# Optimization experiments

Hardware: AMD Instinct MI355X
Metric: run time of the kernel (lower is better)

## Reference

```python
import jax, jax.numpy as jnp
import numpy as np

D_MODEL = 1024; D_STATE = 128; D_CONV = 4; EXPAND = 2; HEADDIM = 64; NGROUPS = 1
CHUNK = 256; B_SZ = 2; SEQ = 4096
D_INNER = EXPAND * D_MODEL
NHEADS = D_INNER // HEADDIM
CONV_DIM = D_INNER + 2 * NGROUPS * D_STATE
D_IN_PROJ = 2 * D_INNER + 2 * NGROUPS * D_STATE + NHEADS
EPS = 1e-5


def setup_inputs() -> dict:
    key = jax.random.key(0)
    ks = jax.random.split(key, 12)
    # dt_bias init exactly as in the module (inverse-softplus of dt in [dt_min, dt_max])
    dt0 = jnp.exp(jax.random.uniform(ks[0], (NHEADS,)) * (np.log(0.1) - np.log(0.001)) + np.log(0.001))
    dt0 = jnp.clip(dt0, 1e-4)
    dt_bias = dt0 + jnp.log(-jnp.expm1(-dt0))
    A_log = jnp.log(jax.random.uniform(ks[1], (NHEADS,), minval=1.0, maxval=16.0))
    return {
        "u": jax.random.normal(ks[2], (B_SZ, SEQ, D_MODEL), jnp.float32),
        "delta_t": jax.random.uniform(ks[3], (B_SZ, SEQ, 1), jnp.float32),
        "W_in": jax.random.normal(ks[4], (D_IN_PROJ, D_MODEL), jnp.float32) / np.sqrt(D_MODEL),
        "conv_w": jax.random.normal(ks[5], (CONV_DIM, D_CONV), jnp.float32) * 0.2,
        "conv_b": jax.random.normal(ks[6], (CONV_DIM,), jnp.float32) * 0.02,
        "dt_bias": dt_bias,
        "gamma": jax.random.uniform(ks[7], (NHEADS,)),
        "A_log": A_log,
        "D": jnp.ones((NHEADS,), jnp.float32),
        "norm_w": jnp.ones((D_INNER,), jnp.float32),
        "W_out": jax.random.normal(ks[8], (D_MODEL, D_INNER), jnp.float32) / np.sqrt(D_INNER),
    }


def _segsum(x):
    # x: (..., T) -> (..., T, T) masked lower-triangular segment sums
    T = x.shape[-1]
    cs = jnp.cumsum(x, axis=-1)
    seg = cs[..., :, None] - cs[..., None, :]
    mask = jnp.tril(jnp.ones((T, T), bool))
    return jnp.where(mask, seg, -jnp.inf)


def _forward(u, delta_t, W_in, conv_w, conv_b, dt_bias, gamma, A_log, D, norm_w, W_out):
    b, L, _ = u.shape
    zxbcdt = u @ W_in.T                               # (b, L, d_in_proj), d_mlp == 0
    z = zxbcdt[..., :D_INNER]
    xBC = zxbcdt[..., D_INNER:D_INNER + CONV_DIM]
    dt = zxbcdt[..., D_INNER + CONV_DIM:]             # (b, L, nheads)
    dt = dt + gamma[None, None, :] * delta_t          # time-scale-aware shift
    # causal depthwise conv1d (pad left d_conv-1) + SiLU
    xBC = jax.lax.conv_general_dilated(
        xBC.transpose(0, 2, 1), conv_w[:, None, :], (1,), [(D_CONV - 1, 0)],
        feature_group_count=CONV_DIM, dimension_numbers=("NCH", "OIH", "NCH"))
    xBC = jax.nn.silu(xBC.transpose(0, 2, 1) + conv_b)
    x = xBC[..., :D_INNER].reshape(b, L, NHEADS, HEADDIM)
    Bm = xBC[..., D_INNER:D_INNER + D_STATE]          # ngroups == 1 -> (b, L, n)
    Cm = xBC[..., D_INNER + D_STATE:]
    A = -jnp.exp(A_log)                               # (h,)
    dt = jax.nn.softplus(dt + dt_bias)                # dt_softplus=True, dt_limit=(0, inf)
    # ---- chunked SSD scan (mamba_chunk_scan_combined) ----
    c = L // CHUNK
    Xc = (x * dt[..., None]).reshape(b, c, CHUNK, NHEADS, HEADDIM)
    Ac = (dt * A).reshape(b, c, CHUNK, NHEADS).transpose(0, 3, 1, 2)    # (b,h,c,Q)
    Bc = Bm.reshape(b, c, CHUNK, D_STATE)
    Cc = Cm.reshape(b, c, CHUNK, D_STATE)
    A_cumsum = jnp.cumsum(Ac, axis=-1)                                   # (b,h,c,Q)
    Lmat = jnp.exp(_segsum(Ac))                                          # (b,h,c,Q,Q)
    # intra-chunk (diagonal blocks)
    Y_diag = jnp.einsum("bcqn,bckn,bhcqk,bckhp->bcqhp", Cc, Bc, Lmat, Xc)
    # per-chunk states at chunk ends
    decay_states = jnp.exp(A_cumsum[..., -1:] - A_cumsum)                # (b,h,c,Q)
    states = jnp.einsum("bckn,bhck,bckhp->bchpn", Bc, decay_states, Xc)
    # inter-chunk recurrence over chunk index
    chunk_decay = jnp.exp(A_cumsum[..., -1])                             # (b,h,c)

    def step(s, inp):
        dec, st = inp
        return dec[..., None, None] * s + st, s

    _, prev_states = jax.lax.scan(
        step,
        jnp.zeros((b, NHEADS, HEADDIM, D_STATE), Xc.dtype),
        (chunk_decay.transpose(2, 0, 1), states.transpose(1, 0, 2, 3, 4)))  # prev: (c,b,h,p,n)
    Y_off = jnp.einsum("bcqn,cbhpn,bhcq->bcqhp", Cc, prev_states, jnp.exp(A_cumsum))
    y = (Y_diag + Y_off).reshape(b, L, NHEADS, HEADDIM)
    y = y + x * D[None, None, :, None]                # skip connection D
    y = y.reshape(b, L, D_INNER)
    # gated RMSNorm (norm_before_gate=False): norm(y * silu(z)) * w, group_size = d_ssm
    yg = y * jax.nn.silu(z)
    yg = yg * jax.lax.rsqrt(jnp.mean(jnp.square(yg), axis=-1, keepdims=True) + EPS) * norm_w
    return yg @ W_out.T


def reference(u, delta_t, W_in, conv_w, conv_b, dt_bias, gamma, A_log, D, norm_w, W_out):
    return _forward(u, delta_t, W_in, conv_w, conv_b, dt_bias, gamma, A_log, D, norm_w, W_out)
```

## Files before the change

kernel.cpp:

```cpp
#include <hip/hip_runtime.h>
#include <hip/hip_bf16.h>
#include <math.h>

#define DM    1024
#define DIP   4384
#define NP1   4480
#define NPX   4352
#define DI    2048
#define CD    2304
#define NH    32
#define HD    64
#define DS    128
#define CH    256
#define NCH   16
#define BSZ   2
#define SEQ   4096
#define NTOK  (BSZ*SEQ)

typedef __bf16 bf16_t;
typedef __attribute__((ext_vector_type(8))) __bf16 bf16x8;
typedef __attribute__((ext_vector_type(4))) float f32x4;

__device__ __forceinline__ f32x4 mfma16(bf16x8 a, bf16x8 b, f32x4 c) {
    return __builtin_amdgcn_mfma_f32_16x16x32_bf16(a, b, c, 0, 0, 0);
}

__device__ __forceinline__ void gload_lds16(const bf16_t* g, bf16_t* l) {
    __builtin_amdgcn_global_load_lds(
        (const __attribute__((address_space(1))) unsigned int*)g,
        (__attribute__((address_space(3))) unsigned int*)l, 16, 0, 0);
}

#define CVT_U   (NTOK * DM)
#define CVT_WI  (NP1 * DM)
#define CVT_WO  (DM * DI)
__global__ void k_cvt_all(const float* __restrict__ u, const float* __restrict__ wi,
                          const float* __restrict__ wo,
                          bf16_t* __restrict__ u_bf, bf16_t* __restrict__ wi_bf,
                          bf16_t* __restrict__ wo_bf) {
    int i = blockIdx.x * 256 + threadIdx.x;
    if (i < CVT_U) {
        u_bf[i] = (bf16_t)u[i];
    } else if (i < CVT_U + CVT_WI) {
        int j = i - CVT_U;
        int r = j >> 10;
        wi_bf[j] = (r < DIP) ? (bf16_t)wi[j] : (bf16_t)0.f;
    } else if (i < CVT_U + CVT_WI + CVT_WO) {
        int j = i - CVT_U - CVT_WI;
        wo_bf[j] = (bf16_t)wo[j];
    }
}

template <typename OutT>
__global__ __launch_bounds__(256) void k_gemm(const bf16_t* __restrict__ A,
                                              const bf16_t* __restrict__ Bt,
                                              OutT* __restrict__ C, int K, int ldc) {
    __shared__ __align__(16) bf16_t sA[128 * 32];
    __shared__ __align__(16) bf16_t sB[128 * 32];
    int tid = threadIdx.x, wave = tid >> 6, lane = tid & 63;
    int l15 = lane & 15, quad = lane >> 4;
    int m0 = blockIdx.y * 128, n0 = blockIdx.x * 128;
    int wm = (wave & 1) * 64, wn = (wave >> 1) * 64;
    f32x4 acc[4][4];
#pragma unroll
    for (int i = 0; i < 4; i++)
#pragma unroll
        for (int j = 0; j < 4; j++) acc[i][j] = (f32x4){0.f, 0.f, 0.f, 0.f};

    int srow = lane >> 2, sc = lane & 3;
    int scol = (sc ^ ((srow >> 1) & 3)) * 8;
    const bf16_t* Ag0 = A + (size_t)(m0 + wave * 32 + srow) * K + scol;
    const bf16_t* Ag1 = Ag0 + (size_t)16 * K;
    const bf16_t* Bg0 = Bt + (size_t)(n0 + wave * 32 + srow) * K + scol;
    const bf16_t* Bg1 = Bg0 + (size_t)16 * K;
    bf16_t* lA0 = sA + (wave * 32) * 32;
    bf16_t* lA1 = sA + (wave * 32 + 16) * 32;
    bf16_t* lB0 = sB + (wave * 32) * 32;
    bf16_t* lB1 = sB + (wave * 32 + 16) * 32;
    int rchunk = (quad ^ ((l15 >> 1) & 3)) * 8;

    for (int k0 = 0; k0 < K; k0 += 32) {
        gload_lds16(Ag0 + k0, lA0);
        gload_lds16(Ag1 + k0, lA1);
        gload_lds16(Bg0 + k0, lB0);
        gload_lds16(Bg1 + k0, lB1);
        __syncthreads();
        bf16x8 af[4], bg[4];
#pragma unroll
        for (int mt = 0; mt < 4; mt++) af[mt] = *(const bf16x8*)&sA[(wm + mt * 16 + l15) * 32 + rchunk];
#pragma unroll
        for (int nt = 0; nt < 4; nt++) bg[nt] = *(const bf16x8*)&sB[(wn + nt * 16 + l15) * 32 + rchunk];
#pragma unroll
        for (int mt = 0; mt < 4; mt++)
#pragma unroll
            for (int nt = 0; nt < 4; nt++)
                acc[mt][nt] = mfma16(af[mt], bg[nt], acc[mt][nt]);
        __syncthreads();
    }
#pragma unroll
    for (int mt = 0; mt < 4; mt++)
#pragma unroll
        for (int nt = 0; nt < 4; nt++)
#pragma unroll
            for (int r = 0; r < 4; r++)
                C[(size_t)(m0 + wm + mt * 16 + quad * 4 + r) * ldc + n0 + wn + nt * 16 + l15] =
                    (OutT)acc[mt][nt][r];
}

#define WPAD 1032
__global__ __launch_bounds__(256) void k_dtgemm(const bf16_t* __restrict__ A,
                                                const bf16_t* __restrict__ Wdt,
                                                float* __restrict__ dtf) {
    __shared__ __align__(16) bf16_t sW[32 * WPAD];
    __shared__ __align__(16) bf16_t sA[128 * 32];
    int tid = threadIdx.x, wave = tid >> 6, lane = tid & 63;
    int l15 = lane & 15, quad = lane >> 4;
    int m0 = blockIdx.x * 128;
#pragma unroll
    for (int it = 0; it < 16; it++) {
        int idx = it * 2048 + tid * 8;
        int r = idx >> 10, c = idx & 1023;
        *(bf16x8*)&sW[r * WPAD + c] = *(const bf16x8*)(Wdt + (size_t)r * DM + c);
    }
    f32x4 acc[2][2];
#pragma unroll
    for (int i = 0; i < 2; i++)
#pragma unroll
        for (int j = 0; j < 2; j++) acc[i][j] = (f32x4){0.f, 0.f, 0.f, 0.f};

    int srow = lane >> 2, sc = lane & 3;
    int scol = (sc ^ ((srow >> 1) & 3)) * 8;
    const bf16_t* Ag0 = A + (size_t)(m0 + wave * 32 + srow) * DM + scol;
    const bf16_t* Ag1 = Ag0 + (size_t)16 * DM;
    bf16_t* lA0 = sA + (wave * 32) * 32;
    bf16_t* lA1 = sA + (wave * 32 + 16) * 32;
    int rchunk = (quad ^ ((l15 >> 1) & 3)) * 8;

    for (int k0 = 0; k0 < DM; k0 += 32) {
        gload_lds16(Ag0 + k0, lA0);
        gload_lds16(Ag1 + k0, lA1);
        __syncthreads();
        bf16x8 af[2], bg[2];
#pragma unroll
        for (int mt = 0; mt < 2; mt++)
            af[mt] = *(const bf16x8*)&sA[(wave * 32 + mt * 16 + l15) * 32 + rchunk];
#pragma unroll
        for (int nt = 0; nt < 2; nt++)
            bg[nt] = *(const bf16x8*)&sW[(nt * 16 + l15) * WPAD + k0 + quad * 8];
#pragma unroll
        for (int mt = 0; mt < 2; mt++)
#pragma unroll
            for (int nt = 0; nt < 2; nt++)
                acc[mt][nt] = mfma16(af[mt], bg[nt], acc[mt][nt]);
        __syncthreads();
    }
#pragma unroll
    for (int mt = 0; mt < 2; mt++)
#pragma unroll
        for (int nt = 0; nt < 2; nt++)
#pragma unroll
            for (int r = 0; r < 4; r++)
                dtf[(size_t)(m0 + wave * 32 + mt * 16 + quad * 4 + r) * NH + nt * 16 + l15] =
                    acc[mt][nt][r];
}

__global__ __launch_bounds__(256) void k_dtcum(const float* __restrict__ dtf,
                                               const float* __restrict__ delta_t,
                                               const float* __restrict__ gamma,
                                               const float* __restrict__ dt_bias,
                                               const float* __restrict__ A_log,
                                               float* __restrict__ dtb, float* __restrict__ acum) {
    int blk = blockIdx.x;
    int h = blk & (NH - 1), bc = blk >> 5;
    int q = threadIdx.x;
    size_t tok = (size_t)bc * CH + q;
    float x = dtf[tok * NH + h] + gamma[h] * delta_t[tok] + dt_bias[h];
    float dt = (x > 20.f) ? x : log1pf(expf(x));
    float Ah = -expf(A_log[h]);
    __shared__ __align__(16) float s[CH];
    s[q] = dt * Ah;
    __syncthreads();
#pragma unroll
    for (int off = 1; off < CH; off <<= 1) {
        float v = (q >= off) ? s[q - off] : 0.f;
        __syncthreads();
        s[q] += v;
        __syncthreads();
    }
    dtb[(size_t)blk * CH + q] = dt;
    acum[(size_t)blk * CH + q] = s[q];
}

__global__ __launch_bounds__(256) void k_conv(const bf16_t* __restrict__ zxp,
                                              const float* __restrict__ cw,
                                              const float* __restrict__ cb,
                                              bf16_t* __restrict__ xBC) {
    int ch = blockIdx.x * 256 + threadIdx.x;
    int tok0 = blockIdx.y * 8;
    int l0 = tok0 & (SEQ - 1);
    float w0 = cw[ch * 4], w1 = cw[ch * 4 + 1], w2 = cw[ch * 4 + 2], w3 = cw[ch * 4 + 3];
    float bias = cb[ch];
    float h0 = 0.f, h1 = 0.f, h2 = 0.f;
    if (l0 != 0) {
        h0 = (float)zxp[(size_t)(tok0 - 3) * NPX + ch];
        h1 = (float)zxp[(size_t)(tok0 - 2) * NPX + ch];
        h2 = (float)zxp[(size_t)(tok0 - 1) * NPX + ch];
    }
#pragma unroll
    for (int j = 0; j < 8; j++) {
        float cur = (float)zxp[(size_t)(tok0 + j) * NPX + ch];
        float acc = bias + h0 * w0 + h1 * w1 + h2 * w2 + cur * w3;
        float sv = acc / (1.f + expf(-acc));
        xBC[(size_t)(tok0 + j) * CD + ch] = (bf16_t)sv;
        h0 = h1; h1 = h2; h2 = cur;
    }
}

__global__ __launch_bounds__(256) void k_trans(const bf16_t* __restrict__ xBC,
                                               const float* __restrict__ dtb,
                                               bf16_t* __restrict__ Xt, bf16_t* __restrict__ Btr) {
    int t = blockIdx.x, bc = blockIdx.y, tid = threadIdx.x;
    __shared__ __align__(16) bf16_t tile[CH][72];
    __shared__ __align__(16) float sdt[CH];
    int chbase = (t < 32) ? t * 64 : DI + (t - 32) * 64;
#pragma unroll
    for (int pp = 0; pp < 8; pp++) {
        int q = pp * 32 + (tid >> 3), col = (tid & 7) * 8;
        *(bf16x8*)&tile[q][col] = *(const bf16x8*)(xBC + (size_t)(bc * CH + q) * CD + chbase + col);
    }
    if (t < 32) sdt[tid] = dtb[(size_t)(bc * NH + t) * CH + tid];
    __syncthreads();
    int pl = tid >> 2, qg = tid & 3;
#pragma unroll
    for (int c8 = 0; c8 < 8; c8++) {
        int q0 = qg * 64 + c8 * 8;
        bf16x8 v;
        if (t < 32) {
#pragma unroll
            for (int j = 0; j < 8; j++) v[j] = (bf16_t)((float)tile[q0 + j][pl] * sdt[q0 + j]);
            size_t row = (size_t)(bc * NH + t) * 64 + pl;
            *(bf16x8*)(Xt + row * CH + q0) = v;
        } else {
#pragma unroll
            for (int j = 0; j < 8; j++) v[j] = tile[q0 + j][pl];
            size_t row = (size_t)bc * DS + (t - 32) * 64 + pl;
            *(bf16x8*)(Btr + row * CH + q0) = v;
        }
    }
}

__global__ __launch_bounds__(256) void k_states(const bf16_t* __restrict__ Xt,
                                                const bf16_t* __restrict__ Btr,
                                                const float* __restrict__ acum,
                                                bf16_t* __restrict__ states) {
    int blk = blockIdx.x;
    int bc = blk >> 5;
    int tid = threadIdx.x, wave = tid >> 6, lane = tid & 63;
    int l15 = lane & 15, quad = lane >> 4;
    __shared__ __align__(16) float sdec[CH];
    {
        size_t base = (size_t)blk * CH;
        float al = acum[base + CH - 1];
        sdec[tid] = __expf(al - acum[base + tid]);
    }
    __syncthreads();
    const bf16_t* Xb = Xt + (size_t)blk * 64 * CH;
    const bf16_t* Bb = Btr + (size_t)bc * DS * CH;
    f32x4 acc[4][2];
#pragma unroll
    for (int i = 0; i < 4; i++)
#pragma unroll
        for (int j = 0; j < 2; j++) acc[i][j] = (f32x4){0.f, 0.f, 0.f, 0.f};
#pragma unroll
    for (int ks = 0; ks < 8; ks++) {
        float d0[8];
#pragma unroll
        for (int j = 0; j < 8; j++) d0[j] = sdec[ks * 32 + quad * 8 + j];
        bf16x8 a[4], b[2];
#pragma unroll
        for (int mt = 0; mt < 4; mt++) {
            bf16x8 raw = *(const bf16x8*)(Xb + (size_t)(mt * 16 + l15) * CH + ks * 32 + quad * 8);
#pragma unroll
            for (int j = 0; j < 8; j++) a[mt][j] = (bf16_t)((float)raw[j] * d0[j]);
        }
#pragma unroll
        for (int nt = 0; nt < 2; nt++)
            b[nt] = *(const bf16x8*)(Bb + (size_t)(wave * 32 + nt * 16 + l15) * CH + ks * 32 + quad * 8);
#pragma unroll
        for (int mt = 0; mt < 4; mt++)
#pragma unroll
            for (int nt = 0; nt < 2; nt++)
                acc[mt][nt] = mfma16(a[mt], b[nt], acc[mt][nt]);
    }
#pragma unroll
    for (int mt = 0; mt < 4; mt++)
#pragma unroll
        for (int nt = 0; nt < 2; nt++)
#pragma unroll
            for (int r = 0; r < 4; r++)
                states[(size_t)blk * 64 * DS + (size_t)(mt * 16 + quad * 4 + r) * DS + wave * 32 + nt * 16 + l15] =
                    (bf16_t)acc[mt][nt][r];
}

__global__ __launch_bounds__(256) void k_scan(const bf16_t* __restrict__ states,
                                              const float* __restrict__ acum,
                                              bf16_t* __restrict__ prevb) {
    int blk = blockIdx.x;
    int bh = blk >> 5;
    int b = bh >> 5, h = bh & 31;
    int e = (blk & 31) * 256 + threadIdx.x;
    float prev = 0.f;
    for (int c = 0; c < NCH; c++) {
        size_t idx = (size_t)(b * NCH + c) * NH + h;
        float dec = __expf(acum[idx * CH + CH - 1]);
        size_t i = idx * 64 * DS + e;
        prevb[i] = (bf16_t)prev;
        prev = prev * dec + (float)states[i];
    }
}

__global__ __launch_bounds__(256) void k_sgen(const bf16_t* __restrict__ xBC,
                                              bf16_t* __restrict__ Sraw) {
    int t = blockIdx.x, bc = blockIdx.y;
    int qt = (t == 0) ? 1 : (t < 3) ? 2 : 3;
    int kt = t - qt * (qt - 1) / 2;
    int tid = threadIdx.x, wave = tid >> 6, lane = tid & 63;
    int l15 = lane & 15, quad = lane >> 4;
    const bf16_t* Cbase = xBC + (size_t)bc * CH * CD + DI + DS;
    const bf16_t* Bbase = xBC + (size_t)bc * CH * CD + DI;
    f32x4 acc[4];
#pragma unroll
    for (int j = 0; j < 4; j++) acc[j] = (f32x4){0.f, 0.f, 0.f, 0.f};
#pragma unroll
    for (int ks = 0; ks < 4; ks++) {
        bf16x8 a = *(const bf16x8*)(Cbase + (size_t)(qt * 64 + wave * 16 + l15) * CD + ks * 32 + quad * 8);
        bf16x8 b[4];
#pragma unroll
        for (int nt = 0; nt < 4; nt++)
            b[nt] = *(const bf16x8*)(Bbase + (size_t)(kt * 64 + nt * 16 + l15) * CD + ks * 32 + quad * 8);
#pragma unroll
        for (int nt = 0; nt < 4; nt++) acc[nt] = mfma16(a, b[nt], acc[nt]);
    }
    bf16_t* out = Sraw + ((size_t)bc * 6 + t) * 64 * 64;
#pragma unroll
    for (int nt = 0; nt < 4; nt++)
#pragma unroll
        for (int r = 0; r < 4; r++)
            out[(size_t)(wave * 16 + quad * 4 + r) * 64 + nt * 16 + l15] = (bf16_t)acc[nt][r];
}

__global__ __launch_bounds__(256) void k_chunky(const bf16_t* __restrict__ xBC,
                                                const bf16_t* __restrict__ Xt,
                                                const bf16_t* __restrict__ prevb,
                                                const bf16_t* __restrict__ Sraw,
                                                const float* __restrict__ acum,
                                                const float* __restrict__ Dp,
                                                bf16_t* __restrict__ yf) {
    int blk = blockIdx.x;
    int bc = blk >> 5, h = blk & 31;
    int tid = threadIdx.x, wave = tid >> 6, lane = tid & 63;
    int l15 = lane & 15, quad = lane >> 4;
    __shared__ __align__(16) float sac[CH];
    __shared__ __align__(16) bf16_t sS[4][64][72];
    sac[tid] = acum[(size_t)blk * CH + tid];
    __syncthreads();

    const bf16_t* Cbase = xBC + (size_t)bc * CH * CD + DI + DS;
    const bf16_t* Bbase = xBC + (size_t)bc * CH * CD + DI;
    const bf16_t* XtB = Xt + (size_t)blk * 64 * CH;
    const bf16_t* pvB = prevb + (size_t)blk * 64 * DS;

    int qw = wave * 64;
    float refq = sac[qw];
    float s_ref = __expf(refq);
    f32x4 acc[4][4];
#pragma unroll
    for (int i = 0; i < 4; i++)
#pragma unroll
        for (int j = 0; j < 4; j++) acc[i][j] = (f32x4){0.f, 0.f, 0.f, 0.f};

#pragma unroll
    for (int ks = 0; ks < 4; ks++) {
        bf16x8 a[4], b[4];
#pragma unroll
        for (int mt = 0; mt < 4; mt++)
            a[mt] = *(const bf16x8*)(Cbase + (size_t)(qw + mt * 16 + l15) * CD + ks * 32 + quad * 8);
#pragma unroll
        for (int nt = 0; nt < 4; nt++)
            b[nt] = *(const bf16x8*)(pvB + (size_t)(nt * 16 + l15) * DS + ks * 32 + quad * 8);
#pragma unroll
        for (int mt = 0; mt < 4; mt++)
#pragma unroll
            for (int nt = 0; nt < 4; nt++)
                acc[mt][nt] = mfma16(a[mt], b[nt], acc[mt][nt]);
    }
#pragma unroll
    for (int mt = 0; mt < 4; mt++)
#pragma unroll
        for (int nt = 0; nt < 4; nt++)
#pragma unroll
            for (int r = 0; r < 4; r++) acc[mt][nt][r] *= s_ref;

    for (int kt = 0; kt < wave; kt++) {
        const bf16_t* St = Sraw + ((size_t)bc * 6 + wave * (wave - 1) / 2 + kt) * 64 * 64;
#pragma unroll
        for (int ks = 0; ks < 2; ks++) {
            float ekv[8];
#pragma unroll
            for (int j = 0; j < 8; j++)
                ekv[j] = __expf(refq - sac[kt * 64 + ks * 32 + quad * 8 + j]);
            bf16x8 a[4], b[4];
#pragma unroll
            for (int mt = 0; mt < 4; mt++)
                a[mt] = *(const bf16x8*)(St + (size_t)(mt * 16 + l15) * 64 + ks * 32 + quad * 8);
#pragma unroll
            for (int nt = 0; nt < 4; nt++) {
                bf16x8 raw = *(const bf16x8*)(XtB + (size_t)(nt * 16 + l15) * CH + kt * 64 + ks * 32 + quad * 8);
#pragma unroll
                for (int j = 0; j < 8; j++) b[nt][j] = (bf16_t)((float)raw[j] * ekv[j]);
            }
#pragma unroll
            for (int mt = 0; mt < 4; mt++)
#pragma unroll
                for (int nt = 0; nt < 4; nt++)
                    acc[mt][nt] = mfma16(a[mt], b[nt], acc[mt][nt]);
        }
    }

    float sacq[4][4];
#pragma unroll
    for (int mt = 0; mt < 4; mt++)
#pragma unroll
        for (int r = 0; r < 4; r++) sacq[mt][r] = sac[qw + mt * 16 + quad * 4 + r];
#pragma unroll
    for (int mt = 0; mt < 4; mt++) {
        float eqv[4];
#pragma unroll
        for (int r = 0; r < 4; r++) eqv[r] = __expf(sacq[mt][r] - refq);
#pragma unroll
        for (int nt = 0; nt < 4; nt++)
#pragma unroll
            for (int r = 0; r < 4; r++) acc[mt][nt][r] *= eqv[r];
    }

    {
        int kt = wave;
        f32x4 s2[4][4];
#pragma unroll
        for (int i = 0; i < 4; i++)
#pragma unroll
            for (int j = 0; j < 4; j++) s2[i][j] = (f32x4){0.f, 0.f, 0.f, 0.f};
#pragma unroll
        for (int ks = 0; ks < 4; ks++) {
            bf16x8 a[4], b[4];
#pragma unroll
            for (int mt = 0; mt < 4; mt++)
                a[mt] = *(const bf16x8*)(Cbase + (size_t)(qw + mt * 16 + l15) * CD + ks * 32 + quad * 8);
#pragma unroll
            for (int nt = 0; nt < 4; nt++)
                b[nt] = *(const bf16x8*)(Bbase + (size_t)(kt * 64 + nt * 16 + l15) * CD + ks * 32 + quad * 8);
#pragma unroll
            for (int mt = 0; mt < 4; mt++)
#pragma unroll
                for (int nt = 0; nt < 4; nt++)
                    s2[mt][nt] = mfma16(a[mt], b[nt], s2[mt][nt]);
        }
        float sack[4];
#pragma unroll
        for (int nt = 0; nt < 4; nt++) sack[nt] = sac[kt * 64 + nt * 16 + l15];
#pragma unroll
        for (int mt = 0; mt < 4; mt++)
#pragma unroll
            for (int nt = 0; nt < 4; nt++) {
                int kp = kt * 64 + nt * 16 + l15;
#pragma unroll
                for (int r = 0; r < 4; r++) {
                    int lq = mt * 16 + quad * 4 + r;
                    int q = qw + lq;
                    float v = (kp <= q) ? s2[mt][nt][r] * __expf(sacq[mt][r] - sack[nt]) : 0.f;
                    sS[wave][lq][nt * 16 + l15] = (bf16_t)v;
                }
            }
#pragma unroll
        for (int ks = 0; ks < 2; ks++) {
            bf16x8 a[4], b[4];
#pragma unroll
            for (int mt = 0; mt < 4; mt++)
                a[mt] = *(const bf16x8*)&sS[wave][mt * 16 + l15][ks * 32 + quad * 8];
#pragma unroll
            for (int nt = 0; nt < 4; nt++)
                b[nt] = *(const bf16x8*)(XtB + (size_t)(nt * 16 + l15) * CH + kt * 64 + ks * 32 + quad * 8);
#pragma unroll
            for (int mt = 0; mt < 4; mt++)
#pragma unroll
                for (int nt = 0; nt < 4; nt++)
                    acc[mt][nt] = mfma16(a[mt], b[nt], acc[mt][nt]);
        }
    }

    float Dh = Dp[h];
#pragma unroll
    for (int mt = 0; mt < 4; mt++)
#pragma unroll
        for (int nt = 0; nt < 4; nt++)
#pragma unroll
            for (int r = 0; r < 4; r++) {
                int q = qw + mt * 16 + quad * 4 + r;
                int p = nt * 16 + l15;
                size_t tok = (size_t)bc * CH + q;
                float xv = (float)xBC[tok * CD + h * 64 + p];
                yf[tok * DI + h * 64 + p] = (bf16_t)(acc[mt][nt][r] + Dh * xv);
            }
}

__global__ __launch_bounds__(256) void k_gate(const bf16_t* __restrict__ yf,
                                              const bf16_t* __restrict__ zb,
                                              const float* __restrict__ nw,
                                              bf16_t* __restrict__ yg) {
    int tok = blockIdx.x, tid = threadIdx.x;
    float g[8];
    float ss = 0.f;
#pragma unroll
    for (int j = 0; j < 8; j++) {
        int d = tid + j * 256;
        float z = (float)zb[(size_t)tok * NPX + d];
        float yy = (float)yf[(size_t)tok * DI + d];
        float gg = yy * (z / (1.f + expf(-z)));
        g[j] = gg;
        ss += gg * gg;
    }
#pragma unroll
    for (int off = 32; off > 0; off >>= 1) ss += __shfl_down(ss, off);
    __shared__ __align__(16) float sw[4];
    int wave = tid >> 6, lane = tid & 63;
    if (lane == 0) sw[wave] = ss;
    __syncthreads();
    float tot = sw[0] + sw[1] + sw[2] + sw[3];
    float r = rsqrtf(tot / (float)DI + 1e-5f);
#pragma unroll
    for (int j = 0; j < 8; j++) {
        int d = tid + j * 256;
        yg[(size_t)tok * DI + d] = (bf16_t)(g[j] * r * nw[d]);
    }
}

extern "C" void kernel_launch(void* const* d_in, const int* in_sizes, int n_in,
                              void* d_out, int out_size, void* d_ws, size_t ws_size,
                              hipStream_t stream) {
    const float* u       = (const float*)d_in[0];
    const float* delta_t = (const float*)d_in[1];
    const float* W_in    = (const float*)d_in[2];
    const float* conv_w  = (const float*)d_in[3];
    const float* conv_b  = (const float*)d_in[4];
    const float* dt_bias = (const float*)d_in[5];
    const float* gamma   = (const float*)d_in[6];
    const float* A_log   = (const float*)d_in[7];
    const float* Dp      = (const float*)d_in[8];
    const float* norm_w  = (const float*)d_in[9];
    const float* W_out   = (const float*)d_in[10];
    float* out = (float*)d_out;

    char* p = (char*)d_ws;
    auto alloc = [&](size_t bytes) -> char* {
        char* r = p;
        p += (bytes + 255) & ~(size_t)255;
        return r;
    };
    bf16_t* zxBC    = (bf16_t*)alloc((size_t)NTOK * NPX * 2);
    bf16_t* Win_bf  = (bf16_t*)alloc((size_t)NP1 * DM * 2);
    bf16_t* Wout_bf = (bf16_t*)alloc((size_t)DM * DI * 2);
    float*  dtb     = (float*)alloc((size_t)NTOK * NH * 4);
    float*  acum    = (float*)alloc((size_t)NTOK * NH * 4);
    bf16_t* xBC_bf  = (bf16_t*)alloc((size_t)NTOK * CD * 2);
    bf16_t* Xt      = (bf16_t*)alloc((size_t)NTOK * DI * 2);
    bf16_t* poolA   = (bf16_t*)alloc((size_t)NTOK * DM * 2);
    bf16_t* Btr     = (bf16_t*)alloc((size_t)BSZ * NCH * DS * CH * 2);
    bf16_t* Sraw    = (bf16_t*)alloc((size_t)BSZ * NCH * 6 * 64 * 64 * 2);
    float*  dtf     = (float*)d_out;
    bf16_t* states  = (bf16_t*)d_out;
    bf16_t* yf      = (bf16_t*)d_out;
    bf16_t* u_bf    = poolA;
    bf16_t* prevb   = poolA;
    bf16_t* yg_bf   = Xt;

    k_cvt_all<<<(CVT_U + CVT_WI + CVT_WO + 255) / 256, 256, 0, stream>>>(
        u, W_in, W_out, u_bf, Win_bf, Wout_bf);

    k_gemm<bf16_t><<<dim3(NPX / 128, NTOK / 128), 256, 0, stream>>>(u_bf, Win_bf, zxBC, DM, NPX);
    k_dtgemm<<<NTOK / 128, 256, 0, stream>>>(u_bf, Win_bf + (size_t)NPX * DM, dtf);

    k_dtcum<<<BSZ * NCH * NH, CH, 0, stream>>>(dtf, delta_t, gamma, dt_bias, A_log, dtb, acum);
    k_conv<<<dim3(CD / 256, NTOK / 8), 256, 0, stream>>>(zxBC + DI, conv_w, conv_b, xBC_bf);
    k_sgen<<<dim3(6, BSZ * NCH), 256, 0, stream>>>(xBC_bf, Sraw);
    k_trans<<<dim3(34, BSZ * NCH), 256, 0, stream>>>(xBC_bf, dtb, Xt, Btr);
    k_states<<<BSZ * NCH * NH, 256, 0, stream>>>(Xt, Btr, acum, states);
    k_scan<<<BSZ * NH * 32, 256, 0, stream>>>(states, acum, prevb);
    k_chunky<<<BSZ * NCH * NH, 256, 0, stream>>>(xBC_bf, Xt, prevb, Sraw, acum, Dp, yf);
    k_gate<<<NTOK, 256, 0, stream>>>(yf, zxBC, norm_w, yg_bf);

    k_gemm<float><<<dim3(DM / 128, NTOK / 128), 256, 0, stream>>>(yg_bf, Wout_bf, out, DI, DM);
}
```

Measured before the change: 463.5 us.

## Widen GEMM K-tile to 64 and merge independent mid-stage kernels

The bf16 GEMM now stages 64-wide K tiles in LDS with an 8-slot XOR swizzle, which halves the number of barriers per K step and doubles the MFMA work done per sync. Separately, the dt-cumsum and conv kernels are merged into one launch via block-index dispatch, and so are the S-generation and transpose kernels, cutting launch count and letting independent work share the machine. The change adds LDS use per block (32 KB), which may lower occupancy. Merged kernels also carry the larger shared footprint of their biggest branch.

```diff
diff --git a/kernel.cpp b/kernel.cpp
--- a/kernel.cpp
+++ b/kernel.cpp
@@ -55,8 +55,8 @@
 __global__ __launch_bounds__(256) void k_gemm(const bf16_t* __restrict__ A,
                                               const bf16_t* __restrict__ Bt,
                                               OutT* __restrict__ C, int K, int ldc) {
-    __shared__ __align__(16) bf16_t sA[128 * 32];
-    __shared__ __align__(16) bf16_t sB[128 * 32];
+    __shared__ __align__(16) bf16_t sA[128 * 64];
+    __shared__ __align__(16) bf16_t sB[128 * 64];
     int tid = threadIdx.x, wave = tid >> 6, lane = tid & 63;
     int l15 = lane & 15, quad = lane >> 4;
     int m0 = blockIdx.y * 128, n0 = blockIdx.x * 128;
@@ -67,34 +67,34 @@
 #pragma unroll
         for (int j = 0; j < 4; j++) acc[i][j] = (f32x4){0.f, 0.f, 0.f, 0.f};
 
-    int srow = lane >> 2, sc = lane & 3;
-    int scol = (sc ^ ((srow >> 1) & 3)) * 8;
-    const bf16_t* Ag0 = A + (size_t)(m0 + wave * 32 + srow) * K + scol;
-    const bf16_t* Ag1 = Ag0 + (size_t)16 * K;
-    const bf16_t* Bg0 = Bt + (size_t)(n0 + wave * 32 + srow) * K + scol;
-    const bf16_t* Bg1 = Bg0 + (size_t)16 * K;
-    bf16_t* lA0 = sA + (wave * 32) * 32;
-    bf16_t* lA1 = sA + (wave * 32 + 16) * 32;
-    bf16_t* lB0 = sB + (wave * 32) * 32;
-    bf16_t* lB1 = sB + (wave * 32 + 16) * 32;
-    int rchunk = (quad ^ ((l15 >> 1) & 3)) * 8;
-
-    for (int k0 = 0; k0 < K; k0 += 32) {
-        gload_lds16(Ag0 + k0, lA0);
-        gload_lds16(Ag1 + k0, lA1);
-        gload_lds16(Bg0 + k0, lB0);
-        gload_lds16(Bg1 + k0, lB1);
+    int srow = lane >> 3, sslot = lane & 7;
+    int scol = (sslot ^ srow) * 8;
+    const bf16_t* Ag = A + (size_t)(m0 + wave * 32 + srow) * K + scol;
+    const bf16_t* Bg = Bt + (size_t)(n0 + wave * 32 + srow) * K + scol;
+    bf16_t* lA = sA + (wave * 32) * 64;
+    bf16_t* lB = sB + (wave * 32) * 64;
+
+    for (int k0 = 0; k0 < K; k0 += 64) {
+#pragma unroll
+        for (int i = 0; i < 4; i++) {
+            gload_lds16(Ag + (size_t)(8 * i) * K + k0, lA + (8 * i) * 64);
+            gload_lds16(Bg + (size_t)(8 * i) * K + k0, lB + (8 * i) * 64);
+        }
         __syncthreads();
-        bf16x8 af[4], bg[4];
-#pragma unroll
-        for (int mt = 0; mt < 4; mt++) af[mt] = *(const bf16x8*)&sA[(wm + mt * 16 + l15) * 32 + rchunk];
-#pragma unroll
-        for (int nt = 0; nt < 4; nt++) bg[nt] = *(const bf16x8*)&sB[(wn + nt * 16 + l15) * 32 + rchunk];
-#pragma unroll
-        for (int mt = 0; mt < 4; mt++)
-#pragma unroll
-            for (int nt = 0; nt < 4; nt++)
-                acc[mt][nt] = mfma16(af[mt], bg[nt], acc[mt][nt]);
+#pragma unroll
+        for (int ks = 0; ks < 2; ks++) {
+            int rslot = ((ks * 4 + quad) ^ (l15 & 7)) * 8;
+            bf16x8 af[4], bg[4];
+#pragma unroll
+            for (int mt = 0; mt < 4; mt++) af[mt] = *(const bf16x8*)&sA[(wm + mt * 16 + l15) * 64 + rslot];
+#pragma unroll
+            for (int nt = 0; nt < 4; nt++) bg[nt] = *(const bf16x8*)&sB[(wn + nt * 16 + l15) * 64 + rslot];
+#pragma unroll
+            for (int mt = 0; mt < 4; mt++)
+#pragma unroll
+                for (int nt = 0; nt < 4; nt++)
+                    acc[mt][nt] = mfma16(af[mt], bg[nt], acc[mt][nt]);
+        }
         __syncthreads();
     }
 #pragma unroll
@@ -164,87 +164,122 @@
                     acc[mt][nt][r];
 }
 
-__global__ __launch_bounds__(256) void k_dtcum(const float* __restrict__ dtf,
-                                               const float* __restrict__ delta_t,
-                                               const float* __restrict__ gamma,
-                                               const float* __restrict__ dt_bias,
-                                               const float* __restrict__ A_log,
-                                               float* __restrict__ dtb, float* __restrict__ acum) {
-    int blk = blockIdx.x;
-    int h = blk & (NH - 1), bc = blk >> 5;
-    int q = threadIdx.x;
-    size_t tok = (size_t)bc * CH + q;
-    float x = dtf[tok * NH + h] + gamma[h] * delta_t[tok] + dt_bias[h];
-    float dt = (x > 20.f) ? x : log1pf(expf(x));
-    float Ah = -expf(A_log[h]);
-    __shared__ __align__(16) float s[CH];
-    s[q] = dt * Ah;
-    __syncthreads();
-#pragma unroll
-    for (int off = 1; off < CH; off <<= 1) {
-        float v = (q >= off) ? s[q - off] : 0.f;
-        __syncthreads();
-        s[q] += v;
-        __syncthreads();
-    }
-    dtb[(size_t)blk * CH + q] = dt;
-    acum[(size_t)blk * CH + q] = s[q];
-}
-
-__global__ __launch_bounds__(256) void k_conv(const bf16_t* __restrict__ zxp,
+__global__ __launch_bounds__(256) void k_mid1(const float* __restrict__ dtf,
+                                              const float* __restrict__ delta_t,
+                                              const float* __restrict__ gamma,
+                                              const float* __restrict__ dt_bias,
+                                              const float* __restrict__ A_log,
+                                              float* __restrict__ dtb, float* __restrict__ acum,
+                                              const bf16_t* __restrict__ zxp,
                                               const float* __restrict__ cw,
                                               const float* __restrict__ cb,
                                               bf16_t* __restrict__ xBC) {
-    int ch = blockIdx.x * 256 + threadIdx.x;
-    int tok0 = blockIdx.y * 8;
-    int l0 = tok0 & (SEQ - 1);
-    float w0 = cw[ch * 4], w1 = cw[ch * 4 + 1], w2 = cw[ch * 4 + 2], w3 = cw[ch * 4 + 3];
-    float bias = cb[ch];
-    float h0 = 0.f, h1 = 0.f, h2 = 0.f;
-    if (l0 != 0) {
-        h0 = (float)zxp[(size_t)(tok0 - 3) * NPX + ch];
-        h1 = (float)zxp[(size_t)(tok0 - 2) * NPX + ch];
-        h2 = (float)zxp[(size_t)(tok0 - 1) * NPX + ch];
-    }
-#pragma unroll
-    for (int j = 0; j < 8; j++) {
-        float cur = (float)zxp[(size_t)(tok0 + j) * NPX + ch];
-        float acc = bias + h0 * w0 + h1 * w1 + h2 * w2 + cur * w3;
-        float sv = acc / (1.f + expf(-acc));
-        xBC[(size_t)(tok0 + j) * CD + ch] = (bf16_t)sv;
-        h0 = h1; h1 = h2; h2 = cur;
-    }
-}
-
-__global__ __launch_bounds__(256) void k_trans(const bf16_t* __restrict__ xBC,
-                                               const float* __restrict__ dtb,
-                                               bf16_t* __restrict__ Xt, bf16_t* __restrict__ Btr) {
-    int t = blockIdx.x, bc = blockIdx.y, tid = threadIdx.x;
-    __shared__ __align__(16) bf16_t tile[CH][72];
-    __shared__ __align__(16) float sdt[CH];
-    int chbase = (t < 32) ? t * 64 : DI + (t - 32) * 64;
-#pragma unroll
-    for (int pp = 0; pp < 8; pp++) {
-        int q = pp * 32 + (tid >> 3), col = (tid & 7) * 8;
-        *(bf16x8*)&tile[q][col] = *(const bf16x8*)(xBC + (size_t)(bc * CH + q) * CD + chbase + col);
-    }
-    if (t < 32) sdt[tid] = dtb[(size_t)(bc * NH + t) * CH + tid];
-    __syncthreads();
-    int pl = tid >> 2, qg = tid & 3;
-#pragma unroll
-    for (int c8 = 0; c8 < 8; c8++) {
-        int q0 = qg * 64 + c8 * 8;
-        bf16x8 v;
-        if (t < 32) {
-#pragma unroll
-            for (int j = 0; j < 8; j++) v[j] = (bf16_t)((float)tile[q0 + j][pl] * sdt[q0 + j]);
-            size_t row = (size_t)(bc * NH + t) * 64 + pl;
-            *(bf16x8*)(Xt + row * CH + q0) = v;
-        } else {
-#pragma unroll
-            for (int j = 0; j < 8; j++) v[j] = tile[q0 + j][pl];
-            size_t row = (size_t)bc * DS + (t - 32) * 64 + pl;
-            *(bf16x8*)(Btr + row * CH + q0) = v;
+    int blk = blockIdx.x;
+    int tid = threadIdx.x;
+    if (blk < 1024) {
+        int h = blk & (NH - 1), bc = blk >> 5;
+        int q = tid;
+        size_t tok = (size_t)bc * CH + q;
+        float x = dtf[tok * NH + h] + gamma[h] * delta_t[tok] + dt_bias[h];
+        float dt = (x > 20.f) ? x : log1pf(expf(x));
+        float Ah = -expf(A_log[h]);
+        __shared__ __align__(16) float s[CH];
+        s[q] = dt * Ah;
+        __syncthreads();
+#pragma unroll
+        for (int off = 1; off < CH; off <<= 1) {
+            float v = (q >= off) ? s[q - off] : 0.f;
+            __syncthreads();
+            s[q] += v;
+            __syncthreads();
+        }
+        dtb[(size_t)blk * CH + q] = dt;
+        acum[(size_t)blk * CH + q] = s[q];
+    } else {
+        int t = blk - 1024;
+        int ch = (t % 9) * 256 + tid;
+        int tok0 = (t / 9) * 8;
+        int l0 = tok0 & (SEQ - 1);
+        float w0 = cw[ch * 4], w1 = cw[ch * 4 + 1], w2 = cw[ch * 4 + 2], w3 = cw[ch * 4 + 3];
+        float bias = cb[ch];
+        float h0 = 0.f, h1 = 0.f, h2 = 0.f;
+        if (l0 != 0) {
+            h0 = (float)zxp[(size_t)(tok0 - 3) * NPX + ch];
+            h1 = (float)zxp[(size_t)(tok0 - 2) * NPX + ch];
+            h2 = (float)zxp[(size_t)(tok0 - 1) * NPX + ch];
+        }
+#pragma unroll
+        for (int j = 0; j < 8; j++) {
+            float cur = (float)zxp[(size_t)(tok0 + j) * NPX + ch];
+            float acc = bias + h0 * w0 + h1 * w1 + h2 * w2 + cur * w3;
+            float sv = acc / (1.f + expf(-acc));
+            xBC[(size_t)(tok0 + j) * CD + ch] = (bf16_t)sv;
+            h0 = h1; h1 = h2; h2 = cur;
+        }
+    }
+}
+
+__global__ __launch_bounds__(256) void k_mid2(const bf16_t* __restrict__ xBC,
+                                              const float* __restrict__ dtb,
+                                              bf16_t* __restrict__ Xt, bf16_t* __restrict__ Btr,
+                                              bf16_t* __restrict__ Sraw) {
+    int blk = blockIdx.x;
+    int tid = threadIdx.x, wave = tid >> 6, lane = tid & 63;
+    int l15 = lane & 15, quad = lane >> 4;
+    if (blk < 192) {
+        int t = blk % 6, bc = blk / 6;
+        int qt = (t == 0) ? 1 : (t < 3) ? 2 : 3;
+        int kt = t - qt * (qt - 1) / 2;
+        const bf16_t* Cbase = xBC + (size_t)bc * CH * CD + DI + DS;
+        const bf16_t* Bbase = xBC + (size_t)bc * CH * CD + DI;
+        f32x4 acc[4];
+#pragma unroll
+        for (int j = 0; j < 4; j++) acc[j] = (f32x4){0.f, 0.f, 0.f, 0.f};
+#pragma unroll
+        for (int ks = 0; ks < 4; ks++) {
+            bf16x8 a = *(const bf16x8*)(Cbase + (size_t)(qt * 64 + wave * 16 + l15) * CD + ks * 32 + quad * 8);
+            bf16x8 b[4];
+#pragma unroll
+            for (int nt = 0; nt < 4; nt++)
+                b[nt] = *(const bf16x8*)(Bbase + (size_t)(kt * 64 + nt * 16 + l15) * CD + ks * 32 + quad * 8);
+#pragma unroll
+            for (int nt = 0; nt < 4; nt++) acc[nt] = mfma16(a, b[nt], acc[nt]);
+        }
+        bf16_t* out = Sraw + ((size_t)bc * 6 + t) * 64 * 64;
+#pragma unroll
+        for (int nt = 0; nt < 4; nt++)
+#pragma unroll
+            for (int r = 0; r < 4; r++)
+                out[(size_t)(wave * 16 + quad * 4 + r) * 64 + nt * 16 + l15] = (bf16_t)acc[nt][r];
+    } else {
+        int tr = blk - 192;
+        int t = tr % 34, bc = tr / 34;
+        __shared__ __align__(16) bf16_t tile[CH][72];
+        __shared__ __align__(16) float sdt[CH];
+        int chbase = (t < 32) ? t * 64 : DI + (t - 32) * 64;
+#pragma unroll
+        for (int pp = 0; pp < 8; pp++) {
+            int q = pp * 32 + (tid >> 3), col = (tid & 7) * 8;
+            *(bf16x8*)&tile[q][col] = *(const bf16x8*)(xBC + (size_t)(bc * CH + q) * CD + chbase + col);
+        }
+        if (t < 32) sdt[tid] = dtb[(size_t)(bc * NH + t) * CH + tid];
+        __syncthreads();
+        int pl = tid >> 2, qg = tid & 3;
+#pragma unroll
+        for (int c8 = 0; c8 < 8; c8++) {
+            int q0 = qg * 64 + c8 * 8;
+            bf16x8 v;
+            if (t < 32) {
+#pragma unroll
+                for (int j = 0; j < 8; j++) v[j] = (bf16_t)((float)tile[q0 + j][pl] * sdt[q0 + j]);
+                size_t row = (size_t)(bc * NH + t) * 64 + pl;
+                *(bf16x8*)(Xt + row * CH + q0) = v;
+            } else {
+#pragma unroll
+                for (int j = 0; j < 8; j++) v[j] = tile[q0 + j][pl];
+                size_t row = (size_t)bc * DS + (t - 32) * 64 + pl;
+                *(bf16x8*)(Btr + row * CH + q0) = v;
+            }
         }
     }
 }
@@ -317,36 +352,6 @@
         prevb[i] = (bf16_t)prev;
         prev = prev * dec + (float)states[i];
     }
-}
-
-__global__ __launch_bounds__(256) void k_sgen(const bf16_t* __restrict__ xBC,
-                                              bf16_t* __restrict__ Sraw) {
-    int t = blockIdx.x, bc = blockIdx.y;
-    int qt = (t == 0) ? 1 : (t < 3) ? 2 : 3;
-    int kt = t - qt * (qt - 1) / 2;
-    int tid = threadIdx.x, wave = tid >> 6, lane = tid & 63;
-    int l15 = lane & 15, quad = lane >> 4;
-    const bf16_t* Cbase = xBC + (size_t)bc * CH * CD + DI + DS;
-    const bf16_t* Bbase = xBC + (size_t)bc * CH * CD + DI;
-    f32x4 acc[4];
-#pragma unroll
-    for (int j = 0; j < 4; j++) acc[j] = (f32x4){0.f, 0.f, 0.f, 0.f};
-#pragma unroll
-    for (int ks = 0; ks < 4; ks++) {
-        bf16x8 a = *(const bf16x8*)(Cbase + (size_t)(qt * 64 + wave * 16 + l15) * CD + ks * 32 + quad * 8);
-        bf16x8 b[4];
-#pragma unroll
-        for (int nt = 0; nt < 4; nt++)
-            b[nt] = *(const bf16x8*)(Bbase + (size_t)(kt * 64 + nt * 16 + l15) * CD + ks * 32 + quad * 8);
-#pragma unroll
-        for (int nt = 0; nt < 4; nt++) acc[nt] = mfma16(a, b[nt], acc[nt]);
-    }
-    bf16_t* out = Sraw + ((size_t)bc * 6 + t) * 64 * 64;
-#pragma unroll
-    for (int nt = 0; nt < 4; nt++)
-#pragma unroll
-        for (int r = 0; r < 4; r++)
-            out[(size_t)(wave * 16 + quad * 4 + r) * 64 + nt * 16 + l15] = (bf16_t)acc[nt][r];
 }
 
 __global__ __launch_bounds__(256) void k_chunky(const bf16_t* __restrict__ xBC,
@@ -589,10 +594,9 @@
     k_gemm<bf16_t><<<dim3(NPX / 128, NTOK / 128), 256, 0, stream>>>(u_bf, Win_bf, zxBC, DM, NPX);
     k_dtgemm<<<NTOK / 128, 256, 0, stream>>>(u_bf, Win_bf + (size_t)NPX * DM, dtf);
 
-    k_dtcum<<<BSZ * NCH * NH, CH, 0, stream>>>(dtf, delta_t, gamma, dt_bias, A_log, dtb, acum);
-    k_conv<<<dim3(CD / 256, NTOK / 8), 256, 0, stream>>>(zxBC + DI, conv_w, conv_b, xBC_bf);
-    k_sgen<<<dim3(6, BSZ * NCH), 256, 0, stream>>>(xBC_bf, Sraw);
-    k_trans<<<dim3(34, BSZ * NCH), 256, 0, stream>>>(xBC_bf, dtb, Xt, Btr);
+    k_mid1<<<1024 + 9 * (NTOK / 8), 256, 0, stream>>>(dtf, delta_t, gamma, dt_bias, A_log,
+                                                      dtb, acum, zxBC + DI, conv_w, conv_b, xBC_bf);
+    k_mid2<<<192 + 34 * BSZ * NCH, 256, 0, stream>>>(xBC_bf, dtb, Xt, Btr, Sraw);
     k_states<<<BSZ * NCH * NH, 256, 0, stream>>>(Xt, Btr, acum, states);
     k_scan<<<BSZ * NH * 32, 256, 0, stream>>>(states, acum, prevb);
     k_chunky<<<BSZ * NCH * NH, 256, 0, stream>>>(xBC_bf, Xt, prevb, Sraw, acum, Dp, yf);
```

After: 442.6 us. 4.5% less time.
